# Kernel optimization log

Measured on AMD Instinct MI355X. Metric: run time of the kernel, lower is better.

The kernel has to match this reference:

```python
import jax, jax.numpy as jnp
import numpy as np

DIM = 1024
DEPTH = 7
PAR = 8
N_NODES = 2 ** (DEPTH + 1) - 1  # 255
WIDTH = PAR * N_NODES  # 2040


def setup_inputs() -> dict:
    key = jax.random.key(0)
    k1, k2, k3, k4 = jax.random.split(key, 4)
    init_k = float(np.sqrt(1.0 / DIM))
    init_k2 = float(np.sqrt(1.0 / ((DEPTH + 1) * PAR)))
    oldx = jax.random.normal(k1, (4, 2048, DIM), dtype=jnp.float32)
    W_in = jax.random.uniform(k2, (WIDTH, DIM), jnp.float32, -init_k, init_k)
    b_in = jax.random.uniform(k3, (WIDTH,), jnp.float32, -init_k, init_k)
    W_out = jax.random.uniform(k4, (DIM, WIDTH), jnp.float32, -init_k2, init_k2)
    return {"oldx": oldx, "W_in": W_in, "b_in": b_in, "W_out": W_out}


def reference(oldx, W_in, b_in, W_out):
    x = oldx.reshape(-1, DIM)                      # [B, dim]
    B = x.shape[0]
    logits = x @ W_in.T + b_in                     # [B, width] dense GEMM over ALL nodes
    decisions = (logits > 0).astype(jnp.int32).reshape(B, PAR, N_NODES)
    acts = jax.nn.silu(logits).reshape(B, PAR, N_NODES)

    # Tree traversal: mark root, then descend DEPTH levels by each node's sign bit.
    current = jnp.zeros((B, PAR), dtype=jnp.int32)
    dmap = jax.nn.one_hot(current, N_NODES, dtype=acts.dtype)  # root node marked
    for d in range(DEPTH):
        cur_platform = 2 ** d - 1
        next_platform = 2 ** (d + 1) - 1
        moves = jnp.take_along_axis(decisions, current[..., None], axis=2)[..., 0]
        current = (current - cur_platform) * 2 + moves + next_platform
        dmap = dmap + jax.nn.one_hot(current, N_NODES, dtype=acts.dtype)

    masked = acts * jax.lax.stop_gradient(dmap)    # only depth+1 nodes per tree survive
    out = masked.reshape(B, WIDTH) @ W_out.T       # [B, dim]
    return out.reshape(oldx.shape)
```

## Files before the change

kernel.cpp:

```cpp
#include <hip/hip_runtime.h>
#include <math.h>

#define DIM 1024
#define DEPTH 7
#define PAR 8
#define N_NODES 255
#define WIDTH 2040
#define MARGIN 0.01f

#define REPLANE(p) ((((p) & 1) << 3) | ((((p) >> 1) & 1) << 4) | ((((p) >> 2) & 1) << 5))

typedef _Float16 half2v __attribute__((ext_vector_type(2)));

__device__ __forceinline__ half2v as_h2(unsigned int u) {
    union { unsigned int u; half2v h; } c; c.u = u; return c.h;
}
__device__ __forceinline__ unsigned int pack_h2(float a, float b) {
    union { half2v h; unsigned int u; } c;
    c.h = (half2v){(_Float16)a, (_Float16)b};
    return c.u;
}

__device__ __forceinline__ float dot2h(unsigned int a, unsigned int b, float c) {
#if __has_builtin(__builtin_amdgcn_fdot2)
    return __builtin_amdgcn_fdot2(as_h2(a), as_h2(b), c, false);
#else
    half2v ha = as_h2(a), hb = as_h2(b);
    c = fmaf((float)ha.x, (float)hb.x, c);
    return fmaf((float)ha.y, (float)hb.y, c);
#endif
}

__device__ __forceinline__ float foldK(float a, float b, int K) {
    const bool hi = (threadIdx.x & (unsigned)K) != 0;
    const float keep = hi ? b : a;
    const float send = hi ? a : b;
    return keep + __shfl_xor(send, K, 64);
}

#define TRANS_BLOCKS 512

__global__ __launch_bounds__(256) void prep_kernel(
    const float* __restrict__ W_out,
    const float* __restrict__ W_in,
    unsigned short* __restrict__ WoT,
    unsigned int* __restrict__ Wh)
{
    __shared__ float tile[64][65];
    if (blockIdx.x < TRANS_BLOCKS) {
        const int w0 = (int)(blockIdx.x & 31) * 64;
        const int d0 = (int)(blockIdx.x >> 5) * 64;
        const int tid = (int)threadIdx.x;
        const int sub = tid & 15;
        const int grp = tid >> 4;

        #pragma unroll
        for (int pass = 0; pass < 4; ++pass) {
            const int dl = pass * 16 + grp;
            const int wl = sub * 4;
            const int w = w0 + wl;
            const int d = d0 + dl;
            float4 v = make_float4(0.f, 0.f, 0.f, 0.f);
            if (w + 3 < WIDTH) {
                v = *(const float4*)(W_out + (size_t)d * WIDTH + w);
            } else {
                float t0 = (w + 0 < WIDTH) ? W_out[(size_t)d * WIDTH + w + 0] : 0.f;
                float t1 = (w + 1 < WIDTH) ? W_out[(size_t)d * WIDTH + w + 1] : 0.f;
                float t2 = (w + 2 < WIDTH) ? W_out[(size_t)d * WIDTH + w + 2] : 0.f;
                float t3 = (w + 3 < WIDTH) ? W_out[(size_t)d * WIDTH + w + 3] : 0.f;
                v = make_float4(t0, t1, t2, t3);
            }
            tile[dl][wl + 0] = v.x; tile[dl][wl + 1] = v.y;
            tile[dl][wl + 2] = v.z; tile[dl][wl + 3] = v.w;
        }
        __syncthreads();
        #pragma unroll
        for (int pass = 0; pass < 4; ++pass) {
            const int wl = pass * 16 + grp;
            const int dl = sub * 4;
            const int w = w0 + wl;
            if (w < WIDTH) {
                uint2 pk;
                pk.x = pack_h2(tile[dl + 0][wl], tile[dl + 1][wl]);
                pk.y = pack_h2(tile[dl + 2][wl], tile[dl + 3][wl]);
                *(uint2*)(WoT + (size_t)w * DIM + d0 + dl) = pk;
            }
        }
    } else {
        const int n4 = WIDTH * DIM / 4;
        const int nthr = ((int)gridDim.x - TRANS_BLOCKS) * 256;
        for (int i = ((int)blockIdx.x - TRANS_BLOCKS) * 256 + (int)threadIdx.x;
             i < n4; i += nthr) {
            float4 v = ((const float4*)W_in)[i];
            uint2 pk;
            pk.x = pack_h2(v.x, v.y);
            pk.y = pack_h2(v.z, v.w);
            ((uint2*)Wh)[i] = pk;
        }
    }
}

__global__ __launch_bounds__(256) void fff_stage1_kernel(
    const float* __restrict__ x,
    const float* __restrict__ W_in,
    const float* __restrict__ b_in,
    const unsigned int* __restrict__ Wh,
    float* __restrict__ acts,
    unsigned short* __restrict__ gidx_out,
    int B)
{
    const int wave = (int)((blockIdx.x * blockDim.x + threadIdx.x) >> 6);
    const int lane = (int)(threadIdx.x & 63);
    if (wave >= B) return;

    const float* xr = x + (size_t)wave * DIM;
    unsigned int xp[8];
    {
        float4 a0 = *(const float4*)(xr + lane * 8 + 0);
        float4 a1 = *(const float4*)(xr + lane * 8 + 4);
        float4 a2 = *(const float4*)(xr + 512 + lane * 8 + 0);
        float4 a3 = *(const float4*)(xr + 512 + lane * 8 + 4);
        xp[0] = pack_h2(a0.x, a0.y);
        xp[1] = pack_h2(a0.z, a0.w);
        xp[2] = pack_h2(a1.x, a1.y);
        xp[3] = pack_h2(a1.z, a1.w);
        xp[4] = pack_h2(a2.x, a2.y);
        xp[5] = pack_h2(a2.z, a2.w);
        xp[6] = pack_h2(a3.x, a3.y);
        xp[7] = pack_h2(a3.z, a3.w);
    }

    unsigned long long nodes = 0ULL;
    const int myp = ((lane >> 3) & 1) | (((lane >> 4) & 1) << 1) | (((lane >> 5) & 1) << 2);

    #pragma unroll 1
    for (int d = 0; d <= DEPTH; ++d) {
        int gidx[PAR];
        #pragma unroll
        for (int p = 0; p < PAR; ++p) {
            const int np = (int)((nodes >> (8 * p)) & 0xffULL);
            gidx[p] = p * N_NODES + np;
        }

        const int ga = (lane & 8) ? gidx[1] : gidx[0];
        const int gb = (lane & 8) ? gidx[3] : gidx[2];
        const int gc = (lane & 8) ? gidx[5] : gidx[4];
        const int gd = (lane & 8) ? gidx[7] : gidx[6];
        const int ge = (lane & 16) ? gb : ga;
        const int gf = (lane & 16) ? gd : gc;
        const int gmine = (lane & 32) ? gf : ge;
        const float bias = b_in[gmine];

        float partial[PAR];
        #pragma unroll
        for (int p = 0; p < PAR; ++p) {
            const unsigned int* wr = Wh + (size_t)gidx[p] * (DIM / 2);
            const uint4 u0 = *(const uint4*)(wr + lane * 4);
            const uint4 u1 = *(const uint4*)(wr + 256 + lane * 4);
            float s = 0.f;
            s = dot2h(xp[0], u0.x, s);
            s = dot2h(xp[1], u0.y, s);
            s = dot2h(xp[2], u0.z, s);
            s = dot2h(xp[3], u0.w, s);
            s = dot2h(xp[4], u1.x, s);
            s = dot2h(xp[5], u1.y, s);
            s = dot2h(xp[6], u1.z, s);
            s = dot2h(xp[7], u1.w, s);
            partial[p] = s;
        }

        const float c01 = foldK(partial[0], partial[1], 8);
        const float c23 = foldK(partial[2], partial[3], 8);
        const float c45 = foldK(partial[4], partial[5], 8);
        const float c67 = foldK(partial[6], partial[7], 8);
        const float d0f = foldK(c01, c23, 16);
        const float d1f = foldK(c45, c67, 16);
        float e = foldK(d0f, d1f, 32);
        e += __shfl_xor(e, 1, 64);
        e += __shfl_xor(e, 2, 64);
        e += __shfl_xor(e, 4, 64);
        float my = e + bias;

        if (d < DEPTH) {
            const unsigned long long bal = __ballot(fabsf(my) < MARGIN);
            unsigned rm = 0;
            #pragma unroll
            for (int p = 0; p < PAR; ++p)
                rm |= ((unsigned)((bal >> REPLANE(p)) & 1ULL)) << p;
            if (rm) {
                while (rm) {
                    const int p = __builtin_ctz(rm); rm &= (rm - 1u);
                    const int np = (int)((nodes >> (8 * p)) & 0xffULL);
                    const int gi = p * N_NODES + np;
                    const float* wr = W_in + (size_t)gi * DIM;
                    float s = 0.f;
                    #pragma unroll
                    for (int q = 0; q < 4; ++q) {
                        const int off = (q & 1) * 4 + (q >> 1) * 512 + lane * 8;
                        const float4 fx = *(const float4*)(xr + off);
                        const float4 fw = *(const float4*)(wr + off);
                        s = fmaf(fx.x, fw.x, s); s = fmaf(fx.y, fw.y, s);
                        s = fmaf(fx.z, fw.z, s); s = fmaf(fx.w, fw.w, s);
                    }
                    #pragma unroll
                    for (int off = 32; off >= 1; off >>= 1)
                        s += __shfl_xor(s, off, 64);
                    const float lf = s + b_in[gi];
                    my = (myp == p) ? lf : my;
                }
            }
        }

        const float act_mine = my / (1.0f + __expf(-my));
        const unsigned long long pos = __ballot(my > 0.0f);

        if ((lane & 7) == 0) {
            const int slot = (wave << 6) + (d << 3) + myp;
            acts[slot] = act_mine;
            gidx_out[slot] = (unsigned short)gmine;
        }

        if (d < DEPTH) {
            #pragma unroll
            for (int p = 0; p < PAR; ++p) {
                const int np = (int)((nodes >> (8 * p)) & 0xffULL);
                const unsigned long long nn = (unsigned long long)
                    (2 * np + 1 + (int)((pos >> REPLANE(p)) & 1ULL));
                nodes = (nodes & ~(0xffULL << (8 * p))) | (nn << (8 * p));
            }
        }
    }
}

__global__ __launch_bounds__(256) void fff_stage2_kernel(
    const float* __restrict__ acts,
    const unsigned short* __restrict__ gidx16,
    const unsigned short* __restrict__ WoT,
    float* __restrict__ out,
    int B)
{
    const int wave = (int)((blockIdx.x * blockDim.x + threadIdx.x) >> 6);
    const int lane = (int)(threadIdx.x & 63);
    if (wave >= B) return;

    const int base = wave << 6;
    const float a_l = acts[base + lane];
    const int   g_l = (int)gidx16[base + lane];

    float acc[16];
    #pragma unroll
    for (int i = 0; i < 16; ++i) acc[i] = 0.f;

    #pragma unroll 4
    for (int e = 0; e < 64; ++e) {
        const float a_ = __shfl(a_l, e, 64);
        const int   g  = __shfl(g_l, e, 64);
        const unsigned short* wo = WoT + (size_t)g * DIM;
        const uint4 u0 = *(const uint4*)(wo + lane * 8);
        const uint4 u1 = *(const uint4*)(wo + 512 + lane * 8);
        half2v h_;
        h_ = as_h2(u0.x); acc[0]  = fmaf((float)h_.x, a_, acc[0]);  acc[1]  = fmaf((float)h_.y, a_, acc[1]);
        h_ = as_h2(u0.y); acc[2]  = fmaf((float)h_.x, a_, acc[2]);  acc[3]  = fmaf((float)h_.y, a_, acc[3]);
        h_ = as_h2(u0.z); acc[4]  = fmaf((float)h_.x, a_, acc[4]);  acc[5]  = fmaf((float)h_.y, a_, acc[5]);
        h_ = as_h2(u0.w); acc[6]  = fmaf((float)h_.x, a_, acc[6]);  acc[7]  = fmaf((float)h_.y, a_, acc[7]);
        h_ = as_h2(u1.x); acc[8]  = fmaf((float)h_.x, a_, acc[8]);  acc[9]  = fmaf((float)h_.y, a_, acc[9]);
        h_ = as_h2(u1.y); acc[10] = fmaf((float)h_.x, a_, acc[10]); acc[11] = fmaf((float)h_.y, a_, acc[11]);
        h_ = as_h2(u1.z); acc[12] = fmaf((float)h_.x, a_, acc[12]); acc[13] = fmaf((float)h_.y, a_, acc[13]);
        h_ = as_h2(u1.w); acc[14] = fmaf((float)h_.x, a_, acc[14]); acc[15] = fmaf((float)h_.y, a_, acc[15]);
    }

    float* orow = out + (size_t)wave * DIM;
    *(float4*)(orow + lane * 8 + 0)       = make_float4(acc[0],  acc[1],  acc[2],  acc[3]);
    *(float4*)(orow + lane * 8 + 4)       = make_float4(acc[4],  acc[5],  acc[6],  acc[7]);
    *(float4*)(orow + 512 + lane * 8 + 0) = make_float4(acc[8],  acc[9],  acc[10], acc[11]);
    *(float4*)(orow + 512 + lane * 8 + 4) = make_float4(acc[12], acc[13], acc[14], acc[15]);
}

__global__ __launch_bounds__(256) void fff_f16_kernel(
    const float* __restrict__ x,
    const float* __restrict__ W_in,
    const float* __restrict__ b_in,
    const unsigned int* __restrict__ Wh,
    const unsigned short* __restrict__ WoT,
    float* __restrict__ out,
    int B)
{
    const int wave = (int)((blockIdx.x * blockDim.x + threadIdx.x) >> 6);
    const int lane = (int)(threadIdx.x & 63);
    if (wave >= B) return;

    const float* xr = x + (size_t)wave * DIM;
    unsigned int xp[8];
    {
        float4 a0 = *(const float4*)(xr + lane * 8 + 0);
        float4 a1 = *(const float4*)(xr + lane * 8 + 4);
        float4 a2 = *(const float4*)(xr + 512 + lane * 8 + 0);
        float4 a3 = *(const float4*)(xr + 512 + lane * 8 + 4);
        xp[0] = pack_h2(a0.x, a0.y);
        xp[1] = pack_h2(a0.z, a0.w);
        xp[2] = pack_h2(a1.x, a1.y);
        xp[3] = pack_h2(a1.z, a1.w);
        xp[4] = pack_h2(a2.x, a2.y);
        xp[5] = pack_h2(a2.z, a2.w);
        xp[6] = pack_h2(a3.x, a3.y);
        xp[7] = pack_h2(a3.z, a3.w);
    }

    float acc[16];
    #pragma unroll
    for (int i = 0; i < 16; ++i) acc[i] = 0.f;

    unsigned long long nodes = 0ULL;
    const int myp = ((lane >> 3) & 1) | (((lane >> 4) & 1) << 1) | (((lane >> 5) & 1) << 2);

    #pragma unroll 1
    for (int d = 0; d <= DEPTH; ++d) {
        int gidx[PAR];
        #pragma unroll
        for (int p = 0; p < PAR; ++p) {
            const int np = (int)((nodes >> (8 * p)) & 0xffULL);
            gidx[p] = p * N_NODES + np;
        }

        const int ga = (lane & 8) ? gidx[1] : gidx[0];
        const int gb = (lane & 8) ? gidx[3] : gidx[2];
        const int gc = (lane & 8) ? gidx[5] : gidx[4];
        const int gd = (lane & 8) ? gidx[7] : gidx[6];
        const int ge = (lane & 16) ? gb : ga;
        const int gf = (lane & 16) ? gd : gc;
        const int gmine = (lane & 32) ? gf : ge;
        const float bias = b_in[gmine];

        float partial[PAR];
        #pragma unroll
        for (int p = 0; p < PAR; ++p) {
            const unsigned int* wr = Wh + (size_t)gidx[p] * (DIM / 2);
            const uint4 u0 = *(const uint4*)(wr + lane * 4);
            const uint4 u1 = *(const uint4*)(wr + 256 + lane * 4);
            float s = 0.f;
            s = dot2h(xp[0], u0.x, s);
            s = dot2h(xp[1], u0.y, s);
            s = dot2h(xp[2], u0.z, s);
            s = dot2h(xp[3], u0.w, s);
            s = dot2h(xp[4], u1.x, s);
            s = dot2h(xp[5], u1.y, s);
            s = dot2h(xp[6], u1.z, s);
            s = dot2h(xp[7], u1.w, s);
            partial[p] = s;
        }

        const float c01 = foldK(partial[0], partial[1], 8);
        const float c23 = foldK(partial[2], partial[3], 8);
        const float c45 = foldK(partial[4], partial[5], 8);
        const float c67 = foldK(partial[6], partial[7], 8);
        const float d0f = foldK(c01, c23, 16);
        const float d1f = foldK(c45, c67, 16);
        float e = foldK(d0f, d1f, 32);
        e += __shfl_xor(e, 1, 64);
        e += __shfl_xor(e, 2, 64);
        e += __shfl_xor(e, 4, 64);
        float my = e + bias;

        if (d < DEPTH) {
            const unsigned long long bal = __ballot(fabsf(my) < MARGIN);
            unsigned rm = 0;
            #pragma unroll
            for (int p = 0; p < PAR; ++p)
                rm |= ((unsigned)((bal >> REPLANE(p)) & 1ULL)) << p;
            if (rm) {
                while (rm) {
                    const int p = __builtin_ctz(rm); rm &= (rm - 1u);
                    const int np = (int)((nodes >> (8 * p)) & 0xffULL);
                    const int gi = p * N_NODES + np;
                    const float* wr = W_in + (size_t)gi * DIM;
                    float s = 0.f;
                    #pragma unroll
                    for (int q = 0; q < 4; ++q) {
                        const int off = (q & 1) * 4 + (q >> 1) * 512 + lane * 8;
                        const float4 fx = *(const float4*)(xr + off);
                        const float4 fw = *(const float4*)(wr + off);
                        s = fmaf(fx.x, fw.x, s); s = fmaf(fx.y, fw.y, s);
                        s = fmaf(fx.z, fw.z, s); s = fmaf(fx.w, fw.w, s);
                    }
                    #pragma unroll
                    for (int off = 32; off >= 1; off >>= 1)
                        s += __shfl_xor(s, off, 64);
                    const float lf = s + b_in[gi];
                    my = (myp == p) ? lf : my;
                }
            }
        }

        const float act_mine = my / (1.0f + __expf(-my));
        const unsigned long long pos = __ballot(my > 0.0f);

        float act[PAR];
        #pragma unroll
        for (int p = 0; p < PAR; ++p)
            act[p] = __shfl(act_mine, REPLANE(p), 64);

        #pragma unroll
        for (int p = 0; p < PAR; ++p) {
            const unsigned short* wo = WoT + (size_t)gidx[p] * DIM;
            const uint4 u0 = *(const uint4*)(wo + lane * 8);
            const uint4 u1 = *(const uint4*)(wo + 512 + lane * 8);
            const float a_ = act[p];
            half2v h_;
            h_ = as_h2(u0.x); acc[0]  = fmaf((float)h_.x, a_, acc[0]);  acc[1]  = fmaf((float)h_.y, a_, acc[1]);
            h_ = as_h2(u0.y); acc[2]  = fmaf((float)h_.x, a_, acc[2]);  acc[3]  = fmaf((float)h_.y, a_, acc[3]);
            h_ = as_h2(u0.z); acc[4]  = fmaf((float)h_.x, a_, acc[4]);  acc[5]  = fmaf((float)h_.y, a_, acc[5]);
            h_ = as_h2(u0.w); acc[6]  = fmaf((float)h_.x, a_, acc[6]);  acc[7]  = fmaf((float)h_.y, a_, acc[7]);
            h_ = as_h2(u1.x); acc[8]  = fmaf((float)h_.x, a_, acc[8]);  acc[9]  = fmaf((float)h_.y, a_, acc[9]);
            h_ = as_h2(u1.y); acc[10] = fmaf((float)h_.x, a_, acc[10]); acc[11] = fmaf((float)h_.y, a_, acc[11]);
            h_ = as_h2(u1.z); acc[12] = fmaf((float)h_.x, a_, acc[12]); acc[13] = fmaf((float)h_.y, a_, acc[13]);
            h_ = as_h2(u1.w); acc[14] = fmaf((float)h_.x, a_, acc[14]); acc[15] = fmaf((float)h_.y, a_, acc[15]);

            if (d < DEPTH) {
                const int np = (int)((nodes >> (8 * p)) & 0xffULL);
                const unsigned long long nn = (unsigned long long)
                    (2 * np + 1 + (int)((pos >> REPLANE(p)) & 1ULL));
                nodes = (nodes & ~(0xffULL << (8 * p))) | (nn << (8 * p));
            }
        }
    }

    float* orow = out + (size_t)wave * DIM;
    *(float4*)(orow + lane * 8 + 0)       = make_float4(acc[0],  acc[1],  acc[2],  acc[3]);
    *(float4*)(orow + lane * 8 + 4)       = make_float4(acc[4],  acc[5],  acc[6],  acc[7]);
    *(float4*)(orow + 512 + lane * 8 + 0) = make_float4(acc[8],  acc[9],  acc[10], acc[11]);
    *(float4*)(orow + 512 + lane * 8 + 4) = make_float4(acc[12], acc[13], acc[14], acc[15]);
}

__global__ __launch_bounds__(256) void fff_fallback_kernel(
    const float* __restrict__ x, const float* __restrict__ W_in,
    const float* __restrict__ b_in, const float* __restrict__ W_out,
    float* __restrict__ out, int B)
{
    const int wave = (int)((blockIdx.x * blockDim.x + threadIdx.x) >> 6);
    const int lane = (int)(threadIdx.x & 63);
    if (wave >= B) return;

    const float* xr = x + (size_t)wave * DIM;
    float4 x4[4];
    x4[0] = *(const float4*)(xr + lane * 8 + 0);
    x4[1] = *(const float4*)(xr + lane * 8 + 4);
    x4[2] = *(const float4*)(xr + 512 + lane * 8 + 0);
    x4[3] = *(const float4*)(xr + 512 + lane * 8 + 4);

    float acc[16];
    #pragma unroll
    for (int i = 0; i < 16; ++i) acc[i] = 0.f;
    int node[PAR];
    #pragma unroll
    for (int p = 0; p < PAR; ++p) node[p] = 0;

    for (int d = 0; d <= DEPTH; ++d) {
        #pragma unroll
        for (int p = 0; p < PAR; ++p) {
            const int gidx = p * N_NODES + node[p];
            const float* wr = W_in + (size_t)gidx * DIM;
            const float4 wa = *(const float4*)(wr + lane * 8 + 0);
            const float4 wb = *(const float4*)(wr + lane * 8 + 4);
            const float4 wc = *(const float4*)(wr + 512 + lane * 8 + 0);
            const float4 wd = *(const float4*)(wr + 512 + lane * 8 + 4);
            float s = 0.f;
            s = fmaf(x4[0].x, wa.x, s); s = fmaf(x4[0].y, wa.y, s);
            s = fmaf(x4[0].z, wa.z, s); s = fmaf(x4[0].w, wa.w, s);
            s = fmaf(x4[1].x, wb.x, s); s = fmaf(x4[1].y, wb.y, s);
            s = fmaf(x4[1].z, wb.z, s); s = fmaf(x4[1].w, wb.w, s);
            s = fmaf(x4[2].x, wc.x, s); s = fmaf(x4[2].y, wc.y, s);
            s = fmaf(x4[2].z, wc.z, s); s = fmaf(x4[2].w, wc.w, s);
            s = fmaf(x4[3].x, wd.x, s); s = fmaf(x4[3].y, wd.y, s);
            s = fmaf(x4[3].z, wd.z, s); s = fmaf(x4[3].w, wd.w, s);
            #pragma unroll
            for (int off = 32; off >= 1; off >>= 1)
                s += __shfl_xor(s, off, 64);
            const float logit = s + b_in[gidx];
            const float act = logit / (1.0f + __expf(-logit));
            #pragma unroll
            for (int k = 0; k < 2; ++k) {
                #pragma unroll
                for (int j = 0; j < 8; ++j) {
                    const int e = k * 512 + lane * 8 + j;
                    acc[k * 8 + j] = fmaf(act, W_out[(size_t)e * WIDTH + gidx], acc[k * 8 + j]);
                }
            }
            node[p] = 2 * node[p] + 1 + ((logit > 0.0f) ? 1 : 0);
        }
    }

    float* orow = out + (size_t)wave * DIM;
    *(float4*)(orow + lane * 8 + 0)       = make_float4(acc[0],  acc[1],  acc[2],  acc[3]);
    *(float4*)(orow + lane * 8 + 4)       = make_float4(acc[4],  acc[5],  acc[6],  acc[7]);
    *(float4*)(orow + 512 + lane * 8 + 0) = make_float4(acc[8],  acc[9],  acc[10], acc[11]);
    *(float4*)(orow + 512 + lane * 8 + 4) = make_float4(acc[12], acc[13], acc[14], acc[15]);
}

extern "C" void kernel_launch(void* const* d_in, const int* in_sizes, int n_in,
                              void* d_out, int out_size, void* d_ws, size_t ws_size,
                              hipStream_t stream) {
    const float* oldx  = (const float*)d_in[0];
    const float* W_in  = (const float*)d_in[1];
    const float* b_in  = (const float*)d_in[2];
    const float* W_out = (const float*)d_in[3];
    float* out = (float*)d_out;

    const int B = in_sizes[0] / DIM;

    const size_t half   = (size_t)WIDTH * DIM * sizeof(unsigned short);
    const size_t actsz  = (size_t)B * 64 * sizeof(float);
    const size_t idxsz  = (size_t)B * 64 * sizeof(unsigned short);
    const bool use_split = (d_ws != nullptr) && (ws_size >= 2 * half + actsz + idxsz);
    const bool use_lp    = (d_ws != nullptr) && (ws_size >= 2 * half);

    const int blocks = (B + 3) / 4;

    if (use_split) {
        unsigned short* WoT  = (unsigned short*)d_ws;
        unsigned int*   Wh   = (unsigned int*)((char*)d_ws + half);
        float*          acts = (float*)((char*)d_ws + 2 * half);
        unsigned short* gidx = (unsigned short*)((char*)d_ws + 2 * half + actsz);
        prep_kernel<<<TRANS_BLOCKS + 1024, 256, 0, stream>>>(W_out, W_in, WoT, Wh);
        fff_stage1_kernel<<<blocks, 256, 0, stream>>>(oldx, W_in, b_in, Wh, acts, gidx, B);
        fff_stage2_kernel<<<blocks, 256, 0, stream>>>(acts, gidx, WoT, out, B);
    } else if (use_lp) {
        unsigned short* WoT = (unsigned short*)d_ws;
        unsigned int*   Wh  = (unsigned int*)((char*)d_ws + half);
        prep_kernel<<<TRANS_BLOCKS + 1024, 256, 0, stream>>>(W_out, W_in, WoT, Wh);
        fff_f16_kernel<<<blocks, 256, 0, stream>>>(oldx, W_in, b_in, Wh, WoT, out, B);
    } else {
        fff_fallback_kernel<<<blocks, 256, 0, stream>>>(oldx, W_in, b_in, W_out, out, B);
    }
}
```

Baseline: 181.1 us.

## Process two rows per wave in stage1 with software-prefetched weight rows

Each wave in the tree-descent stage now handles two batch rows instead of one, interleaving their gather-dot-products, reductions and ballots to expose more independent work per wave. Weight row loads for the next tree are software-prefetched before computing the current one. The launch grid for stage1 is halved accordingly. This is meant to hide gather latency, at the cost of higher register pressure and half as many waves for latency hiding.

```diff
diff --git a/kernel.cpp b/kernel.cpp
--- a/kernel.cpp
+++ b/kernel.cpp
@@ -109,124 +109,207 @@
     unsigned short* __restrict__ gidx_out,
     int B)
 {
-    const int wave = (int)((blockIdx.x * blockDim.x + threadIdx.x) >> 6);
+    const int wv = (int)((blockIdx.x * blockDim.x + threadIdx.x) >> 6);
     const int lane = (int)(threadIdx.x & 63);
-    if (wave >= B) return;
-
-    const float* xr = x + (size_t)wave * DIM;
-    unsigned int xp[8];
+    const int rowA = wv * 2;
+    const int rowB = wv * 2 + 1;
+    if (rowA >= B) return;
+    const bool hasB = (rowB < B);
+
+    const float* xrA = x + (size_t)rowA * DIM;
+    const float* xrB = x + (size_t)(hasB ? rowB : rowA) * DIM;
+
+    unsigned int xpA[8], xpB[8];
     {
-        float4 a0 = *(const float4*)(xr + lane * 8 + 0);
-        float4 a1 = *(const float4*)(xr + lane * 8 + 4);
-        float4 a2 = *(const float4*)(xr + 512 + lane * 8 + 0);
-        float4 a3 = *(const float4*)(xr + 512 + lane * 8 + 4);
-        xp[0] = pack_h2(a0.x, a0.y);
-        xp[1] = pack_h2(a0.z, a0.w);
-        xp[2] = pack_h2(a1.x, a1.y);
-        xp[3] = pack_h2(a1.z, a1.w);
-        xp[4] = pack_h2(a2.x, a2.y);
-        xp[5] = pack_h2(a2.z, a2.w);
-        xp[6] = pack_h2(a3.x, a3.y);
-        xp[7] = pack_h2(a3.z, a3.w);
-    }
-
-    unsigned long long nodes = 0ULL;
+        float4 a0 = *(const float4*)(xrA + lane * 8 + 0);
+        float4 a1 = *(const float4*)(xrA + lane * 8 + 4);
+        float4 a2 = *(const float4*)(xrA + 512 + lane * 8 + 0);
+        float4 a3 = *(const float4*)(xrA + 512 + lane * 8 + 4);
+        xpA[0] = pack_h2(a0.x, a0.y); xpA[1] = pack_h2(a0.z, a0.w);
+        xpA[2] = pack_h2(a1.x, a1.y); xpA[3] = pack_h2(a1.z, a1.w);
+        xpA[4] = pack_h2(a2.x, a2.y); xpA[5] = pack_h2(a2.z, a2.w);
+        xpA[6] = pack_h2(a3.x, a3.y); xpA[7] = pack_h2(a3.z, a3.w);
+        float4 b0 = *(const float4*)(xrB + lane * 8 + 0);
+        float4 b1 = *(const float4*)(xrB + lane * 8 + 4);
+        float4 b2 = *(const float4*)(xrB + 512 + lane * 8 + 0);
+        float4 b3 = *(const float4*)(xrB + 512 + lane * 8 + 4);
+        xpB[0] = pack_h2(b0.x, b0.y); xpB[1] = pack_h2(b0.z, b0.w);
+        xpB[2] = pack_h2(b1.x, b1.y); xpB[3] = pack_h2(b1.z, b1.w);
+        xpB[4] = pack_h2(b2.x, b2.y); xpB[5] = pack_h2(b2.z, b2.w);
+        xpB[6] = pack_h2(b3.x, b3.y); xpB[7] = pack_h2(b3.z, b3.w);
+    }
+
+    unsigned long long nodesA = 0ULL, nodesB = 0ULL;
     const int myp = ((lane >> 3) & 1) | (((lane >> 4) & 1) << 1) | (((lane >> 5) & 1) << 2);
 
     #pragma unroll 1
     for (int d = 0; d <= DEPTH; ++d) {
-        int gidx[PAR];
+        int gA[PAR], gB[PAR];
         #pragma unroll
         for (int p = 0; p < PAR; ++p) {
-            const int np = (int)((nodes >> (8 * p)) & 0xffULL);
-            gidx[p] = p * N_NODES + np;
-        }
-
-        const int ga = (lane & 8) ? gidx[1] : gidx[0];
-        const int gb = (lane & 8) ? gidx[3] : gidx[2];
-        const int gc = (lane & 8) ? gidx[5] : gidx[4];
-        const int gd = (lane & 8) ? gidx[7] : gidx[6];
-        const int ge = (lane & 16) ? gb : ga;
-        const int gf = (lane & 16) ? gd : gc;
-        const int gmine = (lane & 32) ? gf : ge;
-        const float bias = b_in[gmine];
-
-        float partial[PAR];
+            gA[p] = p * N_NODES + (int)((nodesA >> (8 * p)) & 0xffULL);
+            gB[p] = p * N_NODES + (int)((nodesB >> (8 * p)) & 0xffULL);
+        }
+
+        const int gaA = (lane & 8) ? gA[1] : gA[0];
+        const int gbA = (lane & 8) ? gA[3] : gA[2];
+        const int gcA = (lane & 8) ? gA[5] : gA[4];
+        const int gdA = (lane & 8) ? gA[7] : gA[6];
+        const int geA = (lane & 16) ? gbA : gaA;
+        const int gfA = (lane & 16) ? gdA : gcA;
+        const int gmineA = (lane & 32) ? gfA : geA;
+        const float biasA = b_in[gmineA];
+        const int gaB = (lane & 8) ? gB[1] : gB[0];
+        const int gbB = (lane & 8) ? gB[3] : gB[2];
+        const int gcB = (lane & 8) ? gB[5] : gB[4];
+        const int gdB = (lane & 8) ? gB[7] : gB[6];
+        const int geB = (lane & 16) ? gbB : gaB;
+        const int gfB = (lane & 16) ? gdB : gcB;
+        const int gmineB = (lane & 32) ? gfB : geB;
+        const float biasB = b_in[gmineB];
+
+        float pA[PAR], pB[PAR];
+        uint4 a0, a1, b0, b1;
+        {
+            const unsigned int* wrA = Wh + (size_t)gA[0] * (DIM / 2);
+            a0 = *(const uint4*)(wrA + lane * 4);
+            a1 = *(const uint4*)(wrA + 256 + lane * 4);
+            const unsigned int* wrB = Wh + (size_t)gB[0] * (DIM / 2);
+            b0 = *(const uint4*)(wrB + lane * 4);
+            b1 = *(const uint4*)(wrB + 256 + lane * 4);
+        }
         #pragma unroll
         for (int p = 0; p < PAR; ++p) {
-            const unsigned int* wr = Wh + (size_t)gidx[p] * (DIM / 2);
-            const uint4 u0 = *(const uint4*)(wr + lane * 4);
-            const uint4 u1 = *(const uint4*)(wr + 256 + lane * 4);
+            uint4 na0 = a0, na1 = a1, nb0 = b0, nb1 = b1;
+            if (p < PAR - 1) {
+                const unsigned int* wrA = Wh + (size_t)gA[p + 1] * (DIM / 2);
+                na0 = *(const uint4*)(wrA + lane * 4);
+                na1 = *(const uint4*)(wrA + 256 + lane * 4);
+                const unsigned int* wrB = Wh + (size_t)gB[p + 1] * (DIM / 2);
+                nb0 = *(const uint4*)(wrB + lane * 4);
+                nb1 = *(const uint4*)(wrB + 256 + lane * 4);
+            }
             float s = 0.f;
-            s = dot2h(xp[0], u0.x, s);
-            s = dot2h(xp[1], u0.y, s);
-            s = dot2h(xp[2], u0.z, s);
-            s = dot2h(xp[3], u0.w, s);
-            s = dot2h(xp[4], u1.x, s);
-            s = dot2h(xp[5], u1.y, s);
-            s = dot2h(xp[6], u1.z, s);
-            s = dot2h(xp[7], u1.w, s);
-            partial[p] = s;
-        }
-
-        const float c01 = foldK(partial[0], partial[1], 8);
-        const float c23 = foldK(partial[2], partial[3], 8);
-        const float c45 = foldK(partial[4], partial[5], 8);
-        const float c67 = foldK(partial[6], partial[7], 8);
-        const float d0f = foldK(c01, c23, 16);
-        const float d1f = foldK(c45, c67, 16);
-        float e = foldK(d0f, d1f, 32);
-        e += __shfl_xor(e, 1, 64);
-        e += __shfl_xor(e, 2, 64);
-        e += __shfl_xor(e, 4, 64);
-        float my = e + bias;
+            s = dot2h(xpA[0], a0.x, s);
+            s = dot2h(xpA[1], a0.y, s);
+            s = dot2h(xpA[2], a0.z, s);
+            s = dot2h(xpA[3], a0.w, s);
+            s = dot2h(xpA[4], a1.x, s);
+            s = dot2h(xpA[5], a1.y, s);
+            s = dot2h(xpA[6], a1.z, s);
+            s = dot2h(xpA[7], a1.w, s);
+            pA[p] = s;
+            float t = 0.f;
+            t = dot2h(xpB[0], b0.x, t);
+            t = dot2h(xpB[1], b0.y, t);
+            t = dot2h(xpB[2], b0.z, t);
+            t = dot2h(xpB[3], b0.w, t);
+            t = dot2h(xpB[4], b1.x, t);
+            t = dot2h(xpB[5], b1.y, t);
+            t = dot2h(xpB[6], b1.z, t);
+            t = dot2h(xpB[7], b1.w, t);
+            pB[p] = t;
+            a0 = na0; a1 = na1; b0 = nb0; b1 = nb1;
+        }
+
+        const float cA01 = foldK(pA[0], pA[1], 8);
+        const float cB01 = foldK(pB[0], pB[1], 8);
+        const float cA23 = foldK(pA[2], pA[3], 8);
+        const float cB23 = foldK(pB[2], pB[3], 8);
+        const float cA45 = foldK(pA[4], pA[5], 8);
+        const float cB45 = foldK(pB[4], pB[5], 8);
+        const float cA67 = foldK(pA[6], pA[7], 8);
+        const float cB67 = foldK(pB[6], pB[7], 8);
+        const float dA0 = foldK(cA01, cA23, 16);
+        const float dB0 = foldK(cB01, cB23, 16);
+        const float dA1 = foldK(cA45, cA67, 16);
+        const float dB1 = foldK(cB45, cB67, 16);
+        float eA = foldK(dA0, dA1, 32);
+        float eB = foldK(dB0, dB1, 32);
+        eA += __shfl_xor(eA, 1, 64);  eB += __shfl_xor(eB, 1, 64);
+        eA += __shfl_xor(eA, 2, 64);  eB += __shfl_xor(eB, 2, 64);
+        eA += __shfl_xor(eA, 4, 64);  eB += __shfl_xor(eB, 4, 64);
+        float myA = eA + biasA;
+        float myB = eB + biasB;
 
         if (d < DEPTH) {
-            const unsigned long long bal = __ballot(fabsf(my) < MARGIN);
-            unsigned rm = 0;
+            const unsigned long long balA = __ballot(fabsf(myA) < MARGIN);
+            unsigned rmA = 0;
             #pragma unroll
             for (int p = 0; p < PAR; ++p)
-                rm |= ((unsigned)((bal >> REPLANE(p)) & 1ULL)) << p;
-            if (rm) {
-                while (rm) {
-                    const int p = __builtin_ctz(rm); rm &= (rm - 1u);
-                    const int np = (int)((nodes >> (8 * p)) & 0xffULL);
-                    const int gi = p * N_NODES + np;
-                    const float* wr = W_in + (size_t)gi * DIM;
-                    float s = 0.f;
-                    #pragma unroll
-                    for (int q = 0; q < 4; ++q) {
-                        const int off = (q & 1) * 4 + (q >> 1) * 512 + lane * 8;
-                        const float4 fx = *(const float4*)(xr + off);
-                        const float4 fw = *(const float4*)(wr + off);
-                        s = fmaf(fx.x, fw.x, s); s = fmaf(fx.y, fw.y, s);
-                        s = fmaf(fx.z, fw.z, s); s = fmaf(fx.w, fw.w, s);
-                    }
-                    #pragma unroll
-                    for (int off = 32; off >= 1; off >>= 1)
-                        s += __shfl_xor(s, off, 64);
-                    const float lf = s + b_in[gi];
-                    my = (myp == p) ? lf : my;
+                rmA |= ((unsigned)((balA >> REPLANE(p)) & 1ULL)) << p;
+            while (rmA) {
+                const int p = __builtin_ctz(rmA); rmA &= (rmA - 1u);
+                const int gi = p * N_NODES + (int)((nodesA >> (8 * p)) & 0xffULL);
+                const float* wr = W_in + (size_t)gi * DIM;
+                float s = 0.f;
+                #pragma unroll
+                for (int q = 0; q < 4; ++q) {
+                    const int off = (q & 1) * 4 + (q >> 1) * 512 + lane * 8;
+                    const float4 fx = *(const float4*)(xrA + off);
+                    const float4 fw = *(const float4*)(wr + off);
+                    s = fmaf(fx.x, fw.x, s); s = fmaf(fx.y, fw.y, s);
+                    s = fmaf(fx.z, fw.z, s); s = fmaf(fx.w, fw.w, s);
                 }
-            }
-        }
-
-        const float act_mine = my / (1.0f + __expf(-my));
-        const unsigned long long pos = __ballot(my > 0.0f);
+                #pragma unroll
+                for (int off = 32; off >= 1; off >>= 1)
+                    s += __shfl_xor(s, off, 64);
+                const float lf = s + b_in[gi];
+                myA = (myp == p) ? lf : myA;
+            }
+            const unsigned long long balB = __ballot(fabsf(myB) < MARGIN);
+            unsigned rmB = 0;
+            #pragma unroll
+            for (int p = 0; p < PAR; ++p)
+                rmB |= ((unsigned)((balB >> REPLANE(p)) & 1ULL)) << p;
+            while (rmB) {
+                const int p = __builtin_ctz(rmB); rmB &= (rmB - 1u);
+                const int gi = p * N_NODES + (int)((nodesB >> (8 * p)) & 0xffULL);
+                const float* wr = W_in + (size_t)gi * DIM;
+                float s = 0.f;
+                #pragma unroll
+                for (int q = 0; q < 4; ++q) {
+                    const int off = (q & 1) * 4 + (q >> 1) * 512 + lane * 8;
+                    const float4 fx = *(const float4*)(xrB + off);
+                    const float4 fw = *(const float4*)(wr + off);
+                    s = fmaf(fx.x, fw.x, s); s = fmaf(fx.y, fw.y, s);
+                    s = fmaf(fx.z, fw.z, s); s = fmaf(fx.w, fw.w, s);
+                }
+                #pragma unroll
+                for (int off = 32; off >= 1; off >>= 1)
+                    s += __shfl_xor(s, off, 64);
+                const float lf = s + b_in[gi];
+                myB = (myp == p) ? lf : myB;
+            }
+        }
+
+        const float actA = myA / (1.0f + __expf(-myA));
+        const float actB = myB / (1.0f + __expf(-myB));
+        const unsigned long long posA = __ballot(myA > 0.0f);
+        const unsigned long long posB = __ballot(myB > 0.0f);
 
         if ((lane & 7) == 0) {
-            const int slot = (wave << 6) + (d << 3) + myp;
-            acts[slot] = act_mine;
-            gidx_out[slot] = (unsigned short)gmine;
+            const int slotA = (rowA << 6) + (d << 3) + myp;
+            acts[slotA] = actA;
+            gidx_out[slotA] = (unsigned short)gmineA;
+            if (hasB) {
+                const int slotB = (rowB << 6) + (d << 3) + myp;
+                acts[slotB] = actB;
+                gidx_out[slotB] = (unsigned short)gmineB;
+            }
         }
 
         if (d < DEPTH) {
             #pragma unroll
             for (int p = 0; p < PAR; ++p) {
-                const int np = (int)((nodes >> (8 * p)) & 0xffULL);
-                const unsigned long long nn = (unsigned long long)
-                    (2 * np + 1 + (int)((pos >> REPLANE(p)) & 1ULL));
-                nodes = (nodes & ~(0xffULL << (8 * p))) | (nn << (8 * p));
+                const int npA = (int)((nodesA >> (8 * p)) & 0xffULL);
+                const unsigned long long nnA = (unsigned long long)
+                    (2 * npA + 1 + (int)((posA >> REPLANE(p)) & 1ULL));
+                nodesA = (nodesA & ~(0xffULL << (8 * p))) | (nnA << (8 * p));
+                const int npB = (int)((nodesB >> (8 * p)) & 0xffULL);
+                const unsigned long long nnB = (unsigned long long)
+                    (2 * npB + 1 + (int)((posB >> REPLANE(p)) & 1ULL));
+                nodesB = (nodesB & ~(0xffULL << (8 * p))) | (nnB << (8 * p));
             }
         }
     }
@@ -521,7 +604,9 @@
         float*          acts = (float*)((char*)d_ws + 2 * half);
         unsigned short* gidx = (unsigned short*)((char*)d_ws + 2 * half + actsz);
         prep_kernel<<<TRANS_BLOCKS + 1024, 256, 0, stream>>>(W_out, W_in, WoT, Wh);
-        fff_stage1_kernel<<<blocks, 256, 0, stream>>>(oldx, W_in, b_in, Wh, acts, gidx, B);
+        const int wavesS1 = (B + 1) / 2;
+        const int blocksS1 = (wavesS1 + 3) / 4;
+        fff_stage1_kernel<<<blocksS1, 256, 0, stream>>>(oldx, W_in, b_in, Wh, acts, gidx, B);
         fff_stage2_kernel<<<blocks, 256, 0, stream>>>(acts, gidx, WoT, out, B);
     } else if (use_lp) {
         unsigned short* WoT = (unsigned short*)d_ws;
```

Measured after the change: 179.1 us. Within noise of the previous version (-1.1%).
